# Performance work log

Hardware: AMD Instinct MI355X
Metric: run time of the kernel (lower is better)

The kernel has to match this reference:

```python
import jax, jax.numpy as jnp
import numpy as np

N_NODES = 100000
IN_F = 512
OUT_F = 512
N_EDGES = 3200000


def setup_inputs() -> dict:
    key = jax.random.key(0)
    k1, k2, k3, k4, k5 = jax.random.split(key, 5)
    features = jax.random.normal(k1, (N_NODES, IN_F), dtype=jnp.float32)
    # xavier_uniform: bound = sqrt(6/(in+out))
    bound = np.sqrt(6.0 / (IN_F + OUT_F)).astype(np.float32)
    weight = jax.random.uniform(k2, (IN_F, OUT_F), dtype=jnp.float32,
                                minval=-bound, maxval=bound)
    edge_row = jax.random.randint(k3, (N_EDGES,), 0, N_NODES, dtype=jnp.int32)
    edge_col = jax.random.randint(k4, (N_EDGES,), 0, N_NODES, dtype=jnp.int32)
    # normalized-adjacency-like positive values
    edge_val = jax.random.uniform(k5, (N_EDGES,), dtype=jnp.float32)
    return {"features": features, "weight": weight, "edge_row": edge_row,
            "edge_col": edge_col, "edge_val": edge_val}


def reference(features, weight, edge_row, edge_col, edge_val):
    # support = features @ W   (dense GEMM, [N, out])
    support = features @ weight
    # output = spmm(adj, support): out[r] += val * support[c] for each edge (r, c)
    messages = edge_val[:, None] * support[edge_col]          # [E, out]
    output = jax.ops.segment_sum(messages, edge_row, num_segments=N_NODES)
    # active=True branch: fused ReLU
    return jax.nn.relu(output)
```

## Files before the change

kernel.cpp:

```cpp
#include <hip/hip_runtime.h>
#include <hip/hip_bf16.h>

#define N_NODES 100000
#define M_PAD   100096
#define FDIM    512
#define N_EDGES 3200000
#define SCAN_BLOCKS 98
#define GEMM_BLOCKS 3128
#define GEMM_MAIN   3104

typedef __attribute__((ext_vector_type(8))) short short8;
typedef __attribute__((ext_vector_type(8))) unsigned short ushort8;
typedef __attribute__((ext_vector_type(4))) unsigned short ushort4_t;
typedef __attribute__((ext_vector_type(4))) float floatx4;
typedef __attribute__((ext_vector_type(2))) int intx2;

__device__ __forceinline__ unsigned short f2bf(float f) {
    unsigned u = __float_as_uint(f);
    u += 0x7FFFu + ((u >> 16) & 1u);
    return (unsigned short)(u >> 16);
}
__device__ __forceinline__ float bf2f(unsigned short u) {
    return __uint_as_float(((unsigned)u) << 16);
}

__global__ __launch_bounds__(256) void convert_w_k(const float* __restrict__ W,
                                                   unsigned short* __restrict__ Wt) {
    int idx = blockIdx.x * 256 + threadIdx.x;
    int k = idx >> 9, n = idx & 511;
    Wt[n * 512 + k] = f2bf(W[idx]);
}

__global__ __launch_bounds__(256) void convert_a_k(const float* __restrict__ F,
                                                   unsigned short* __restrict__ Af) {
    int i = blockIdx.x * 256 + threadIdx.x;
    if (i >= (N_NODES * FDIM) / 8) return;
    const float4* p = (const float4*)F + (size_t)i * 2;
    float4 a = p[0], b = p[1];
    ushort8 u = { f2bf(a.x), f2bf(a.y), f2bf(a.z), f2bf(a.w),
                  f2bf(b.x), f2bf(b.y), f2bf(b.z), f2bf(b.w) };
    *(ushort8*)(Af + (size_t)i * 8) = u;
}

__global__ __launch_bounds__(256) void zero_counts_k(int* __restrict__ counts) {
    int i = blockIdx.x * 256 + threadIdx.x;
    if (i < N_NODES) counts[i] = 0;
}

__global__ __launch_bounds__(256) void hist_k(const int* __restrict__ row,
                                              int* __restrict__ counts) {
    int i = blockIdx.x * 256 + threadIdx.x;
    if (i < N_EDGES) atomicAdd(&counts[row[i]], 1);
}

__global__ __launch_bounds__(1024) void scan1_k(const int* __restrict__ counts,
                                                int* __restrict__ row_start,
                                                int* __restrict__ bsum) {
    __shared__ int sm[1024];
    const int b = blockIdx.x, tid = threadIdx.x;
    const int i = b * 1024 + tid;
    int v = (i < N_NODES) ? counts[i] : 0;
    sm[tid] = v;
    __syncthreads();
    #pragma unroll
    for (int off = 1; off < 1024; off <<= 1) {
        int t = (tid >= off) ? sm[tid - off] : 0;
        __syncthreads();
        sm[tid] += t;
        __syncthreads();
    }
    if (i < N_NODES) row_start[i] = sm[tid] - v;
    if (tid == 1023) bsum[b] = sm[1023];
}

__global__ __launch_bounds__(128) void scan2_k(const int* __restrict__ bsum,
                                               int* __restrict__ boffset) {
    __shared__ int sm[128];
    const int tid = threadIdx.x;
    int v = (tid < SCAN_BLOCKS) ? bsum[tid] : 0;
    sm[tid] = v;
    __syncthreads();
    #pragma unroll
    for (int off = 1; off < 128; off <<= 1) {
        int t = (tid >= off) ? sm[tid - off] : 0;
        __syncthreads();
        sm[tid] += t;
        __syncthreads();
    }
    if (tid < SCAN_BLOCKS) boffset[tid] = sm[tid] - v;
}

__global__ __launch_bounds__(256) void scan3_k(const int* __restrict__ boffset,
                                               int* __restrict__ row_start,
                                               int* __restrict__ cursor) {
    int i = blockIdx.x * 256 + threadIdx.x;
    if (i < N_NODES) {
        int rs = row_start[i] + boffset[i >> 10];
        row_start[i] = rs;
        cursor[i] = rs;
    }
    if (i == 0) row_start[N_NODES] = N_EDGES;
}

__global__ __launch_bounds__(256) void scatter_k(const int* __restrict__ row,
                                                 const int* __restrict__ col,
                                                 const float* __restrict__ val,
                                                 int* __restrict__ cursor,
                                                 int2* __restrict__ edges) {
    int i = blockIdx.x * 256 + threadIdx.x;
    if (i < N_EDGES) {
        int r = row[i];
        int pos = atomicAdd(&cursor[r], 1);
        edges[pos] = make_int2(col[i], __float_as_int(val[i]));
    }
}

__global__ __launch_bounds__(256) void gemm_k(const unsigned short* __restrict__ A,
                                              const unsigned short* __restrict__ Bt,
                                              unsigned short* __restrict__ C) {
    const int id = blockIdx.x;
    int mb, nb;
    if (id < GEMM_MAIN) {
        mb = (id >> 5) * 8 + (id & 7);
        nb = (id >> 3) & 3;
    } else {
        int t = id - GEMM_MAIN;
        mb = 776 + (t >> 2);
        nb = t & 3;
    }
    const int baseM = mb * 128;
    const int baseN = nb * 128;
    const int tid  = threadIdx.x;
    const int lane = tid & 63, wave = tid >> 6;
    const int wm = (wave & 1) * 64;
    const int wn = (wave >> 1) * 64;
    const int lrow = lane & 15, quad = lane >> 4;

    __shared__ unsigned short As[128 * 32];
    __shared__ unsigned short Bs[128 * 32];

    floatx4 acc[4][4] = {};

    for (int k0 = 0; k0 < FDIM; k0 += 32) {
        #pragma unroll
        for (int i = 0; i < 2; ++i) {
            int ofs = i * 4096 + tid * 16;
            int row = ofs >> 6;
            int ke  = (ofs & 63) >> 1;
            __builtin_amdgcn_global_load_lds(
                (const __attribute__((address_space(1))) void*)
                    (A + (size_t)(baseM + row) * FDIM + k0 + ke),
                (__attribute__((address_space(3))) void*)((char*)As + ofs),
                16, 0, 0);
            __builtin_amdgcn_global_load_lds(
                (const __attribute__((address_space(1))) void*)
                    (Bt + (size_t)(baseN + row) * FDIM + k0 + ke),
                (__attribute__((address_space(3))) void*)((char*)Bs + ofs),
                16, 0, 0);
        }
        __syncthreads();

        short8 af[4], bfr[4];
        #pragma unroll
        for (int mi = 0; mi < 4; ++mi)
            af[mi] = *(const short8*)(As + (wm + mi * 16 + lrow) * 32 + quad * 8);
        #pragma unroll
        for (int ni = 0; ni < 4; ++ni)
            bfr[ni] = *(const short8*)(Bs + (wn + ni * 16 + lrow) * 32 + quad * 8);
        #pragma unroll
        for (int mi = 0; mi < 4; ++mi)
            #pragma unroll
            for (int ni = 0; ni < 4; ++ni)
                acc[mi][ni] = __builtin_amdgcn_mfma_f32_16x16x32_bf16(
                    af[mi], bfr[ni], acc[mi][ni], 0, 0, 0);
        __syncthreads();
    }

    #pragma unroll
    for (int mi = 0; mi < 4; ++mi)
        #pragma unroll
        for (int ni = 0; ni < 4; ++ni)
            #pragma unroll
            for (int rr = 0; rr < 4; ++rr) {
                int row  = baseM + wm + mi * 16 + quad * 4 + rr;
                int colj = baseN + wn + ni * 16 + lrow;
                if (row < N_NODES)
                    C[(size_t)row * FDIM + colj] = f2bf(acc[mi][ni][rr]);
            }
}

__global__ __launch_bounds__(64) void spmm_k(const unsigned short* __restrict__ sup,
                                             const int* __restrict__ row_start,
                                             const int2* __restrict__ edges,
                                             float* __restrict__ out) {
    const int r = blockIdx.x;
    const int lane = threadIdx.x;
    const int start = row_start[r], end = row_start[r + 1];
    const unsigned short* supl = sup + lane * 8;

    float acc[8] = {0.f, 0.f, 0.f, 0.f, 0.f, 0.f, 0.f, 0.f};

    const int n8 = (end - start) & ~7;
    for (int eb = start; eb < start + n8; eb += 8) {
        intx2 p[8];
        #pragma unroll
        for (int j = 0; j < 8; ++j)
            p[j] = __builtin_nontemporal_load((const intx2*)&edges[eb + j]);
        ushort8 s[8];
        #pragma unroll
        for (int j = 0; j < 8; ++j)
            s[j] = *(const ushort8*)(supl + (size_t)p[j].x * FDIM);
        #pragma unroll
        for (int j = 0; j < 8; ++j) {
            float v = __int_as_float(p[j].y);
            #pragma unroll
            for (int i = 0; i < 8; ++i)
                acc[i] += v * bf2f((unsigned short)s[j][i]);
        }
    }
    for (int e = start + n8; e < end; ++e) {
        intx2 p = __builtin_nontemporal_load((const intx2*)&edges[e]);
        ushort8 s = *(const ushort8*)(supl + (size_t)p.x * FDIM);
        float v = __int_as_float(p.y);
        #pragma unroll
        for (int i = 0; i < 8; ++i) acc[i] += v * bf2f((unsigned short)s[i]);
    }

    float* op = out + (size_t)r * FDIM + lane * 8;
    floatx4 o0 = { fmaxf(acc[0], 0.f), fmaxf(acc[1], 0.f),
                   fmaxf(acc[2], 0.f), fmaxf(acc[3], 0.f) };
    floatx4 o1 = { fmaxf(acc[4], 0.f), fmaxf(acc[5], 0.f),
                   fmaxf(acc[6], 0.f), fmaxf(acc[7], 0.f) };
    __builtin_nontemporal_store(o0, (floatx4*)op);
    __builtin_nontemporal_store(o1, (floatx4*)(op + 4));
}

extern "C" void kernel_launch(void* const* d_in, const int* in_sizes, int n_in,
                              void* d_out, int out_size, void* d_ws, size_t ws_size,
                              hipStream_t stream) {
    const float* features = (const float*)d_in[0];
    const float* weight   = (const float*)d_in[1];
    const int*   edge_row = (const int*)d_in[2];
    const int*   edge_col = (const int*)d_in[3];
    const float* edge_val = (const float*)d_in[4];
    float* out = (float*)d_out;

    char* ws = (char*)d_ws;
    size_t off = 0;
    unsigned short* sup = (unsigned short*)(ws + off); off += (size_t)N_NODES * FDIM * 2;
    unsigned short* Af  = (unsigned short*)(ws + off); off += (size_t)M_PAD * FDIM * 2;
    unsigned short* Wt  = (unsigned short*)(ws + off); off += (size_t)FDIM * FDIM * 2;
    int* counts    = (int*)(ws + off); off += 400128;
    int* row_start = (int*)(ws + off); off += 400128;
    int* cursor    = (int*)(ws + off); off += 400128;
    int* bsum      = (int*)(ws + off); off += 512;
    int* boffset   = (int*)(ws + off); off += 512;
    int2* edges    = (int2*)(ws + off); off += (size_t)N_EDGES * 8;

    convert_w_k<<<dim3((FDIM * FDIM) / 256), dim3(256), 0, stream>>>(weight, Wt);
    convert_a_k<<<dim3((N_NODES * FDIM / 8 + 255) / 256), dim3(256), 0, stream>>>(features, Af);
    zero_counts_k<<<dim3((N_NODES + 255) / 256), dim3(256), 0, stream>>>(counts);
    hist_k<<<dim3(N_EDGES / 256), dim3(256), 0, stream>>>(edge_row, counts);
    scan1_k<<<dim3(SCAN_BLOCKS), dim3(1024), 0, stream>>>(counts, row_start, bsum);
    scan2_k<<<dim3(1), dim3(128), 0, stream>>>(bsum, boffset);
    scan3_k<<<dim3((N_NODES + 255) / 256), dim3(256), 0, stream>>>(boffset, row_start, cursor);
    scatter_k<<<dim3(N_EDGES / 256), dim3(256), 0, stream>>>(edge_row, edge_col, edge_val,
                                                             cursor, edges);
    gemm_k<<<dim3(GEMM_BLOCKS), dim3(256), 0, stream>>>(Af, Wt, sup);
    spmm_k<<<dim3(N_NODES), dim3(64), 0, stream>>>(sup, row_start, edges, out);
}
```

Baseline: 1.275 ms.

## Replace global-atomic CSR build with two-pass LDS bucket radix sort

Builds the row-sorted edge list with a two-level counting sort. The first pass histograms and scatters edges into coarse buckets of 256 rows using shared-memory atomics per slice. The second pass sorts each bucket by the low 8 bits of the row inside LDS. This replaces per-edge global atomics on 100k counters and cursors, and the temporaries reuse the support buffer before the GEMM writes it. The cost is one extra pass over the edge data and more kernels whose scratch layout depends on fixed sizes.

```diff
diff --git a/kernel.cpp b/kernel.cpp
--- a/kernel.cpp
+++ b/kernel.cpp
@@ -5,9 +5,12 @@
 #define M_PAD   100096
 #define FDIM    512
 #define N_EDGES 3200000
-#define SCAN_BLOCKS 98
 #define GEMM_BLOCKS 3128
 #define GEMM_MAIN   3104
+
+#define NB    391
+#define B1    782
+#define SLICE 4096
 
 typedef __attribute__((ext_vector_type(8))) short short8;
 typedef __attribute__((ext_vector_type(8))) unsigned short ushort8;
@@ -42,24 +45,26 @@
     *(ushort8*)(Af + (size_t)i * 8) = u;
 }
 
-__global__ __launch_bounds__(256) void zero_counts_k(int* __restrict__ counts) {
-    int i = blockIdx.x * 256 + threadIdx.x;
-    if (i < N_NODES) counts[i] = 0;
-}
-
-__global__ __launch_bounds__(256) void hist_k(const int* __restrict__ row,
-                                              int* __restrict__ counts) {
-    int i = blockIdx.x * 256 + threadIdx.x;
-    if (i < N_EDGES) atomicAdd(&counts[row[i]], 1);
-}
-
-__global__ __launch_bounds__(1024) void scan1_k(const int* __restrict__ counts,
-                                                int* __restrict__ row_start,
-                                                int* __restrict__ bsum) {
+__global__ __launch_bounds__(256) void hist1_k(const int* __restrict__ row,
+                                               int* __restrict__ H) {
+    __shared__ int h[NB];
+    const int b = blockIdx.x;
+    for (int k = threadIdx.x; k < NB; k += 256) h[k] = 0;
+    __syncthreads();
+    const int base = b * SLICE;
+    const int limit = min(base + SLICE, N_EDGES);
+    for (int i = base + threadIdx.x; i < limit; i += 256)
+        atomicAdd(&h[row[i] >> 8], 1);
+    __syncthreads();
+    for (int k = threadIdx.x; k < NB; k += 256)
+        H[b * NB + k] = h[k];
+}
+
+__global__ __launch_bounds__(1024) void scanA_k(int* __restrict__ H,
+                                                int* __restrict__ totals) {
     __shared__ int sm[1024];
-    const int b = blockIdx.x, tid = threadIdx.x;
-    const int i = b * 1024 + tid;
-    int v = (i < N_NODES) ? counts[i] : 0;
+    const int k = blockIdx.x, tid = threadIdx.x;
+    int v = (tid < B1) ? H[tid * NB + k] : 0;
     sm[tid] = v;
     __syncthreads();
     #pragma unroll
@@ -69,49 +74,82 @@
         sm[tid] += t;
         __syncthreads();
     }
-    if (i < N_NODES) row_start[i] = sm[tid] - v;
-    if (tid == 1023) bsum[b] = sm[1023];
-}
-
-__global__ __launch_bounds__(128) void scan2_k(const int* __restrict__ bsum,
-                                               int* __restrict__ boffset) {
-    __shared__ int sm[128];
+    if (tid < B1) H[tid * NB + k] = sm[tid] - v;
+    if (tid == B1 - 1) totals[k] = sm[tid];
+}
+
+__global__ __launch_bounds__(512) void scanB_k(const int* __restrict__ totals,
+                                               int* __restrict__ start) {
+    __shared__ int sm[512];
     const int tid = threadIdx.x;
-    int v = (tid < SCAN_BLOCKS) ? bsum[tid] : 0;
+    int v = (tid < NB) ? totals[tid] : 0;
     sm[tid] = v;
     __syncthreads();
     #pragma unroll
-    for (int off = 1; off < 128; off <<= 1) {
+    for (int off = 1; off < 512; off <<= 1) {
         int t = (tid >= off) ? sm[tid - off] : 0;
         __syncthreads();
         sm[tid] += t;
         __syncthreads();
     }
-    if (tid < SCAN_BLOCKS) boffset[tid] = sm[tid] - v;
-}
-
-__global__ __launch_bounds__(256) void scan3_k(const int* __restrict__ boffset,
+    if (tid < NB) start[tid] = sm[tid] - v;
+    if (tid == 0) start[NB] = N_EDGES;
+}
+
+__global__ __launch_bounds__(256) void scatter1_k(const int* __restrict__ row,
+                                                  const int* __restrict__ col,
+                                                  const float* __restrict__ val,
+                                                  const int* __restrict__ H,
+                                                  const int* __restrict__ start,
+                                                  int2* __restrict__ tmp_cv,
+                                                  unsigned char* __restrict__ tmp_r8) {
+    __shared__ int cur[NB];
+    const int b = blockIdx.x;
+    for (int k = threadIdx.x; k < NB; k += 256)
+        cur[k] = start[k] + H[b * NB + k];
+    __syncthreads();
+    const int base = b * SLICE;
+    const int limit = min(base + SLICE, N_EDGES);
+    for (int i = base + threadIdx.x; i < limit; i += 256) {
+        int r = row[i];
+        int p = atomicAdd(&cur[r >> 8], 1);
+        tmp_cv[p] = make_int2(col[i], __float_as_int(val[i]));
+        tmp_r8[p] = (unsigned char)(r & 255);
+    }
+}
+
+__global__ __launch_bounds__(256) void sort2_k(const int* __restrict__ start,
+                                               const int2* __restrict__ tmp_cv,
+                                               const unsigned char* __restrict__ tmp_r8,
                                                int* __restrict__ row_start,
-                                               int* __restrict__ cursor) {
-    int i = blockIdx.x * 256 + threadIdx.x;
-    if (i < N_NODES) {
-        int rs = row_start[i] + boffset[i >> 10];
-        row_start[i] = rs;
-        cursor[i] = rs;
-    }
-    if (i == 0) row_start[N_NODES] = N_EDGES;
-}
-
-__global__ __launch_bounds__(256) void scatter_k(const int* __restrict__ row,
-                                                 const int* __restrict__ col,
-                                                 const float* __restrict__ val,
-                                                 int* __restrict__ cursor,
-                                                 int2* __restrict__ edges) {
-    int i = blockIdx.x * 256 + threadIdx.x;
-    if (i < N_EDGES) {
-        int r = row[i];
-        int pos = atomicAdd(&cursor[r], 1);
-        edges[pos] = make_int2(col[i], __float_as_int(val[i]));
+                                               int2* __restrict__ edges) {
+    __shared__ int h[256];
+    __shared__ int cur[256];
+    const int k = blockIdx.x, tid = threadIdx.x;
+    const int base = start[k], cnt = start[k + 1] - base;
+    h[tid] = 0;
+    __syncthreads();
+    for (int i = tid; i < cnt; i += 256)
+        atomicAdd(&h[tmp_r8[base + i]], 1);
+    __syncthreads();
+    int v = h[tid];
+    #pragma unroll
+    for (int off = 1; off < 256; off <<= 1) {
+        int t = (tid >= off) ? h[tid - off] : 0;
+        __syncthreads();
+        h[tid] += t;
+        __syncthreads();
+    }
+    int excl = h[tid] - v;
+    int r = (k << 8) + tid;
+    if (r < N_NODES) row_start[r] = base + excl;
+    cur[tid] = base + excl;
+    if (k == NB - 1 && tid == 0) row_start[N_NODES] = N_EDGES;
+    __syncthreads();
+    for (int i = tid; i < cnt; i += 256) {
+        unsigned char rl = tmp_r8[base + i];
+        int p = atomicAdd(&cur[rl], 1);
+        edges[p] = tmp_cv[base + i];
     }
 }
 
@@ -250,22 +288,23 @@
     unsigned short* sup = (unsigned short*)(ws + off); off += (size_t)N_NODES * FDIM * 2;
     unsigned short* Af  = (unsigned short*)(ws + off); off += (size_t)M_PAD * FDIM * 2;
     unsigned short* Wt  = (unsigned short*)(ws + off); off += (size_t)FDIM * FDIM * 2;
-    int* counts    = (int*)(ws + off); off += 400128;
     int* row_start = (int*)(ws + off); off += 400128;
-    int* cursor    = (int*)(ws + off); off += 400128;
-    int* bsum      = (int*)(ws + off); off += 512;
-    int* boffset   = (int*)(ws + off); off += 512;
     int2* edges    = (int2*)(ws + off); off += (size_t)N_EDGES * 8;
+    char* supb = (char*)sup;
+    int2* tmp_cv         = (int2*)(supb);
+    unsigned char* tmp_r8 = (unsigned char*)(supb + 25600000);
+    int* H      = (int*)(supb + 28800000);
+    int* totals = (int*)(supb + 30026240);
+    int* startb = (int*)(supb + 30030336);
 
     convert_w_k<<<dim3((FDIM * FDIM) / 256), dim3(256), 0, stream>>>(weight, Wt);
     convert_a_k<<<dim3((N_NODES * FDIM / 8 + 255) / 256), dim3(256), 0, stream>>>(features, Af);
-    zero_counts_k<<<dim3((N_NODES + 255) / 256), dim3(256), 0, stream>>>(counts);
-    hist_k<<<dim3(N_EDGES / 256), dim3(256), 0, stream>>>(edge_row, counts);
-    scan1_k<<<dim3(SCAN_BLOCKS), dim3(1024), 0, stream>>>(counts, row_start, bsum);
-    scan2_k<<<dim3(1), dim3(128), 0, stream>>>(bsum, boffset);
-    scan3_k<<<dim3((N_NODES + 255) / 256), dim3(256), 0, stream>>>(boffset, row_start, cursor);
-    scatter_k<<<dim3(N_EDGES / 256), dim3(256), 0, stream>>>(edge_row, edge_col, edge_val,
-                                                             cursor, edges);
+    hist1_k<<<dim3(B1), dim3(256), 0, stream>>>(edge_row, H);
+    scanA_k<<<dim3(NB), dim3(1024), 0, stream>>>(H, totals);
+    scanB_k<<<dim3(1), dim3(512), 0, stream>>>(totals, startb);
+    scatter1_k<<<dim3(B1), dim3(256), 0, stream>>>(edge_row, edge_col, edge_val,
+                                                   H, startb, tmp_cv, tmp_r8);
+    sort2_k<<<dim3(NB), dim3(256), 0, stream>>>(startb, tmp_cv, tmp_r8, row_start, edges);
     gemm_k<<<dim3(GEMM_BLOCKS), dim3(256), 0, stream>>>(Af, Wt, sup);
     spmm_k<<<dim3(N_NODES), dim3(64), 0, stream>>>(sup, row_start, edges, out);
 }
```

Result: faster. 1.082 ms (-15.1%).
